# Optimization experiments

Hardware: AMD Instinct MI355X
Metric: run time of the kernel (lower is better)

## Reference

```python
import jax, jax.numpy as jnp
import numpy as np

WINDOW = 5  # len_sort_window in the original module


def setup_inputs() -> dict:
    key = jax.random.key(0)
    k1, k2, k3 = jax.random.split(key, 3)
    B, L, D = 8, 4000, 512  # L divisible by WINDOW, D < L
    q = jax.random.normal(k1, (B, L, D), dtype=jnp.float32)
    k = jax.random.normal(k2, (B, L, D), dtype=jnp.float32)
    v = jax.random.normal(k3, (B, L, D), dtype=jnp.float32)
    return {"q": q, "k": k, "v": v}


def reference(q, k, v):
    # q, k are unused by the original forward.
    B, L, D = v.shape
    t = jnp.arange(L)          # sequence positions
    s = jnp.arange(D)          # per-feature cyclic shift amount (= feature index)
    # Shift feature i left by i: shifted[:, t, i] = v[:, (t + i) % L, i]
    idx_fwd = (t[:, None] + s[None, :]) % L            # [L, D]
    v_shift = jnp.take_along_axis(v, idx_fwd[None, :, :], axis=1)  # [B, L, D]
    # Sort within fixed non-overlapping windows of size WINDOW along the seq axis.
    v_sorted = jnp.sort(v_shift.reshape(B, L // WINDOW, WINDOW, D), axis=2)
    v_sorted = v_sorted.reshape(B, L, D)
    # Unshift feature i right by i: out[:, t, i] = v_sorted[:, (t - i) % L, i]
    idx_bwd = (t[:, None] - s[None, :]) % L            # [L, D]
    return jnp.take_along_axis(v_sorted, idx_bwd[None, :, :], axis=1)
```

## Files before the change

### kernel.cpp

```cpp
#include <hip/hip_runtime.h>


constexpr int L = 4000;
constexpr int D = 512;
constexpr int NCG = D / 4;
constexpr int NG  = L / 5;

typedef float vf4 __attribute__((ext_vector_type(4)));

#define CE(a, b) { float lo_ = fminf(a, b); float hi_ = fmaxf(a, b); (a) = lo_; (b) = hi_; }

#define PROC_COL(C, RC)                                                            \
  {                                                                                \
    const bool e0 = (RC) == 0, e1 = (RC) == 1, e2 = (RC) == 2, e3 = (RC) == 3;     \
    float A0 = e0 ? pg[0][C] : e1 ? pg[1][C] : e2 ? pg[2][C] : e3 ? pg[3][C] : pg[4][C];  \
    float A1 = e0 ? pg[1][C] : e1 ? pg[2][C] : e2 ? pg[3][C] : e3 ? pg[4][C] : cg_[0][C]; \
    float A2 = e0 ? pg[2][C] : e1 ? pg[3][C] : e2 ? pg[4][C] : e3 ? cg_[0][C] : cg_[1][C];\
    float A3 = e0 ? pg[3][C] : e1 ? pg[4][C] : e2 ? cg_[0][C] : e3 ? cg_[1][C] : cg_[2][C];\
    float A4 = e0 ? pg[4][C] : e1 ? cg_[0][C] : e2 ? cg_[1][C] : e3 ? cg_[2][C] : cg_[3][C];\
    float B0 = e0 ? cg_[0][C] : e1 ? cg_[1][C] : e2 ? cg_[2][C] : e3 ? cg_[3][C] : cg_[4][C];\
    float B1 = e0 ? cg_[1][C] : e1 ? cg_[2][C] : e2 ? cg_[3][C] : e3 ? cg_[4][C] : ng[0][C]; \
    float B2 = e0 ? cg_[2][C] : e1 ? cg_[3][C] : e2 ? cg_[4][C] : e3 ? ng[0][C] : ng[1][C];  \
    float B3 = e0 ? cg_[3][C] : e1 ? cg_[4][C] : e2 ? ng[0][C] : e3 ? ng[1][C] : ng[2][C];   \
    float B4 = e0 ? cg_[4][C] : e1 ? ng[0][C] : e2 ? ng[1][C] : e3 ? ng[2][C] : ng[3][C];    \
    CE(A0, A1) CE(A3, A4) CE(A2, A4) CE(A2, A3) CE(A1, A4)                         \
    CE(A0, A3) CE(A0, A2) CE(A1, A3) CE(A1, A2)                                    \
    CE(B0, B1) CE(B3, B4) CE(B2, B4) CE(B2, B3) CE(B1, B4)                         \
    CE(B0, B3) CE(B0, B2) CE(B1, B3) CE(B1, B2)                                    \
    fa[0][C] = e0 ? B0 : e1 ? A4 : e2 ? A3 : e3 ? A2 : A1;                         \
    fa[1][C] = e0 ? B1 : e1 ? B0 : e2 ? A4 : e3 ? A3 : A2;                         \
    fa[2][C] = e0 ? B2 : e1 ? B1 : e2 ? B0 : e3 ? A4 : A3;                         \
    fa[3][C] = e0 ? B3 : e1 ? B2 : e2 ? B1 : e3 ? B0 : A4;                         \
    fa[4][C] = e0 ? B4 : e1 ? B3 : e2 ? B2 : e3 ? B1 : B0;                         \
  }

__global__ __launch_bounds__(256)
void swd18_oneshot(const float* __restrict__ v, float* __restrict__ out) {
    const int tid = blockIdx.x * 256 + threadIdx.x;
    const int cg  = tid & (NCG - 1);
    const int rem = tid >> 7;
    const int g   = rem % NG;
    const int b   = rem / NG;

    const float* __restrict__ vb = v   + (size_t)b * (L * D) + cg * 4;
    float*       __restrict__ ob = out + (size_t)b * (L * D) + cg * 4;

    const int r0 = 5 * g;
    int rp = r0 - 5; if (rp < 0)  rp += L;
    int rn = r0 + 5; if (rn >= L) rn -= L;

    vf4 pg[5], cg_[5], ng[5];
#pragma unroll
    for (int j = 0; j < 5; ++j) pg[j]  = *(const vf4*)(vb + (size_t)(rp + j) * D);
#pragma unroll
    for (int j = 0; j < 5; ++j) cg_[j] = *(const vf4*)(vb + (size_t)(r0 + j) * D);
#pragma unroll
    for (int j = 0; j < 5; ++j) ng[j]  = *(const vf4*)(vb + (size_t)(rn + j) * D);

    const int rc0 = (4 * cg) % 5;
    const int rc1 = (rc0 + 1) % 5;
    const int rc2 = (rc0 + 2) % 5;
    const int rc3 = (rc0 + 3) % 5;

    vf4 fa[5];
    PROC_COL(0, rc0)
    PROC_COL(1, rc1)
    PROC_COL(2, rc2)
    PROC_COL(3, rc3)

#pragma unroll
    for (int j = 0; j < 5; ++j)
        __builtin_nontemporal_store(fa[j], (vf4*)(ob + (size_t)(r0 + j) * D));
}

#undef PROC_COL
#undef CE

extern "C" void kernel_launch(void* const* d_in, const int* in_sizes, int n_in,
                              void* d_out, int out_size, void* d_ws, size_t ws_size,
                              hipStream_t stream) {
    const float* v = (const float*)d_in[2];
    float* out = (float*)d_out;

    const int B = in_sizes[2] / (L * D);
    const int nthreads = NCG * NG * B;
    swd18_oneshot<<<dim3(nthreads / 256), dim3(256), 0, stream>>>(v, out);
}
```

Before: 178.9 us.

## Process four window groups per thread to reuse neighbor rows

Each thread now handles a strip of four consecutive 5-row groups, loading 30 rows once instead of 15 rows per group. Neighbouring groups share their previous and next rows in registers, which cuts redundant global loads from three times the data to about 1.5 times. In exchange, register pressure per thread rises, and the grid becomes a 2D launch with far fewer threads, which lowers parallelism and latency hiding.

Measured after the change: 182.9 us. +2.2%, slower.

```diff
diff --git a/kernel.cpp b/kernel.cpp
--- a/kernel.cpp
+++ b/kernel.cpp
@@ -4,7 +4,9 @@
 constexpr int L = 4000;
 constexpr int D = 512;
 constexpr int NCG = D / 4;
-constexpr int NG  = L / 5;
+constexpr int GPT = 4;
+constexpr int SROWS = 5 * GPT;
+constexpr int NSTRIPS = L / SROWS;
 
 typedef float vf4 __attribute__((ext_vector_type(4)));
 
@@ -13,16 +15,16 @@
 #define PROC_COL(C, RC)                                                            \
   {                                                                                \
     const bool e0 = (RC) == 0, e1 = (RC) == 1, e2 = (RC) == 2, e3 = (RC) == 3;     \
-    float A0 = e0 ? pg[0][C] : e1 ? pg[1][C] : e2 ? pg[2][C] : e3 ? pg[3][C] : pg[4][C];  \
-    float A1 = e0 ? pg[1][C] : e1 ? pg[2][C] : e2 ? pg[3][C] : e3 ? pg[4][C] : cg_[0][C]; \
-    float A2 = e0 ? pg[2][C] : e1 ? pg[3][C] : e2 ? pg[4][C] : e3 ? cg_[0][C] : cg_[1][C];\
-    float A3 = e0 ? pg[3][C] : e1 ? pg[4][C] : e2 ? cg_[0][C] : e3 ? cg_[1][C] : cg_[2][C];\
-    float A4 = e0 ? pg[4][C] : e1 ? cg_[0][C] : e2 ? cg_[1][C] : e3 ? cg_[2][C] : cg_[3][C];\
-    float B0 = e0 ? cg_[0][C] : e1 ? cg_[1][C] : e2 ? cg_[2][C] : e3 ? cg_[3][C] : cg_[4][C];\
-    float B1 = e0 ? cg_[1][C] : e1 ? cg_[2][C] : e2 ? cg_[3][C] : e3 ? cg_[4][C] : ng[0][C]; \
-    float B2 = e0 ? cg_[2][C] : e1 ? cg_[3][C] : e2 ? cg_[4][C] : e3 ? ng[0][C] : ng[1][C];  \
-    float B3 = e0 ? cg_[3][C] : e1 ? cg_[4][C] : e2 ? ng[0][C] : e3 ? ng[1][C] : ng[2][C];   \
-    float B4 = e0 ? cg_[4][C] : e1 ? ng[0][C] : e2 ? ng[1][C] : e3 ? ng[2][C] : ng[3][C];    \
+    float A0 = e0 ? pg[0][C] : e1 ? pg[1][C] : e2 ? pg[2][C] : e3 ? pg[3][C] : pg[4][C]; \
+    float A1 = e0 ? pg[1][C] : e1 ? pg[2][C] : e2 ? pg[3][C] : e3 ? pg[4][C] : cu[0][C]; \
+    float A2 = e0 ? pg[2][C] : e1 ? pg[3][C] : e2 ? pg[4][C] : e3 ? cu[0][C] : cu[1][C]; \
+    float A3 = e0 ? pg[3][C] : e1 ? pg[4][C] : e2 ? cu[0][C] : e3 ? cu[1][C] : cu[2][C]; \
+    float A4 = e0 ? pg[4][C] : e1 ? cu[0][C] : e2 ? cu[1][C] : e3 ? cu[2][C] : cu[3][C]; \
+    float B0 = e0 ? cu[0][C] : e1 ? cu[1][C] : e2 ? cu[2][C] : e3 ? cu[3][C] : cu[4][C]; \
+    float B1 = e0 ? cu[1][C] : e1 ? cu[2][C] : e2 ? cu[3][C] : e3 ? cu[4][C] : ng[0][C]; \
+    float B2 = e0 ? cu[2][C] : e1 ? cu[3][C] : e2 ? cu[4][C] : e3 ? ng[0][C] : ng[1][C]; \
+    float B3 = e0 ? cu[3][C] : e1 ? cu[4][C] : e2 ? ng[0][C] : e3 ? ng[1][C] : ng[2][C]; \
+    float B4 = e0 ? cu[4][C] : e1 ? ng[0][C] : e2 ? ng[1][C] : e3 ? ng[2][C] : ng[3][C]; \
     CE(A0, A1) CE(A3, A4) CE(A2, A4) CE(A2, A3) CE(A1, A4)                         \
     CE(A0, A3) CE(A0, A2) CE(A1, A3) CE(A1, A2)                                    \
     CE(B0, B1) CE(B3, B4) CE(B2, B4) CE(B2, B3) CE(B1, B4)                         \
@@ -34,43 +36,47 @@
     fa[4][C] = e0 ? B4 : e1 ? B3 : e2 ? B2 : e3 ? B1 : B0;                         \
   }
 
-__global__ __launch_bounds__(256)
-void swd18_oneshot(const float* __restrict__ v, float* __restrict__ out) {
-    const int tid = blockIdx.x * 256 + threadIdx.x;
-    const int cg  = tid & (NCG - 1);
-    const int rem = tid >> 7;
-    const int g   = rem % NG;
-    const int b   = rem / NG;
+__global__ __launch_bounds__(256, 2)
+void swd18_strip4(const float* __restrict__ v, float* __restrict__ out) {
+    const int cgi   = threadIdx.x & (NCG - 1);
+    const int ls    = threadIdx.x >> 7;
+    const int strip = blockIdx.x * 2 + ls;
+    const int b     = blockIdx.y;
 
-    const float* __restrict__ vb = v   + (size_t)b * (L * D) + cg * 4;
-    float*       __restrict__ ob = out + (size_t)b * (L * D) + cg * 4;
+    const float* __restrict__ vb = v   + (size_t)b * (L * D) + cgi * 4;
+    float*       __restrict__ ob = out + (size_t)b * (L * D) + cgi * 4;
 
-    const int r0 = 5 * g;
-    int rp = r0 - 5; if (rp < 0)  rp += L;
-    int rn = r0 + 5; if (rn >= L) rn -= L;
+    vf4 rows[30];
+#pragma unroll
+    for (int jg = 0; jg < 6; ++jg) {
+        int gb = strip * SROWS - 5 + 5 * jg;
+        if (gb < 0)  gb += L;
+        if (gb >= L) gb -= L;
+#pragma unroll
+        for (int i = 0; i < 5; ++i)
+            rows[5 * jg + i] = *(const vf4*)(vb + (size_t)(gb + i) * D);
+    }
 
-    vf4 pg[5], cg_[5], ng[5];
-#pragma unroll
-    for (int j = 0; j < 5; ++j) pg[j]  = *(const vf4*)(vb + (size_t)(rp + j) * D);
-#pragma unroll
-    for (int j = 0; j < 5; ++j) cg_[j] = *(const vf4*)(vb + (size_t)(r0 + j) * D);
-#pragma unroll
-    for (int j = 0; j < 5; ++j) ng[j]  = *(const vf4*)(vb + (size_t)(rn + j) * D);
-
-    const int rc0 = (4 * cg) % 5;
+    const int rc0 = (4 * cgi) % 5;
     const int rc1 = (rc0 + 1) % 5;
     const int rc2 = (rc0 + 2) % 5;
     const int rc3 = (rc0 + 3) % 5;
 
-    vf4 fa[5];
-    PROC_COL(0, rc0)
-    PROC_COL(1, rc1)
-    PROC_COL(2, rc2)
-    PROC_COL(3, rc3)
-
 #pragma unroll
-    for (int j = 0; j < 5; ++j)
-        __builtin_nontemporal_store(fa[j], (vf4*)(ob + (size_t)(r0 + j) * D));
+    for (int k = 0; k < GPT; ++k) {
+        const vf4* pg = &rows[5 * k];
+        const vf4* cu = &rows[5 * k + 5];
+        const vf4* ng = &rows[5 * k + 10];
+        vf4 fa[5];
+        PROC_COL(0, rc0)
+        PROC_COL(1, rc1)
+        PROC_COL(2, rc2)
+        PROC_COL(3, rc3)
+        const int ro = strip * SROWS + 5 * k;
+#pragma unroll
+        for (int j = 0; j < 5; ++j)
+            __builtin_nontemporal_store(fa[j], (vf4*)(ob + (size_t)(ro + j) * D));
+    }
 }
 
 #undef PROC_COL
@@ -83,6 +89,6 @@
     float* out = (float*)d_out;
 
     const int B = in_sizes[2] / (L * D);
-    const int nthreads = NCG * NG * B;
-    swd18_oneshot<<<dim3(nthreads / 256), dim3(256), 0, stream>>>(v, out);
+    dim3 grid(NSTRIPS / 2, B);
+    swd18_strip4<<<grid, dim3(256), 0, stream>>>(v, out);
 }
```
